# Kernel optimization log

Hardware: AMD Instinct MI355X
Metric: run time of the kernel (lower is better)

Reference implementation:

```python
import jax, jax.numpy as jnp
import numpy as np
import math

B, S, D, H = 4, 1024, 1024, 16
DK = D // H
WINDOW = 128
NEG = -100000.0


def setup_inputs() -> dict:
    key = jax.random.key(0)
    kx, kw1, kb1, kw2, kb2 = jax.random.split(key, 5)
    x = jax.random.normal(kx, (B, S, D), dtype=jnp.float32)
    # sliding-window band mask: True where |i-j| <= WINDOW
    i = jnp.arange(S)
    band = (jnp.abs(i[:, None] - i[None, :]) <= WINDOW)
    mask = jnp.broadcast_to(band, (B, S, S))
    # second structured mask: causal
    causal = (i[:, None] >= i[None, :])
    mask2 = jnp.broadcast_to(causal, (B, S, S))
    scale = 1.0 / math.sqrt(D)
    Wqkv = jax.random.normal(kw1, (D, 3 * D), dtype=jnp.float32) * scale
    bqkv = jax.random.normal(kb1, (3 * D,), dtype=jnp.float32) * 0.01
    Wo = jax.random.normal(kw2, (D, D), dtype=jnp.float32) * scale
    bo = jax.random.normal(kb2, (D,), dtype=jnp.float32) * 0.01
    return {"x": x, "mask": mask, "mask2": mask2, "Wqkv": Wqkv, "bqkv": bqkv, "Wo": Wo, "bo": bo}


def reference(x, mask, mask2, Wqkv, bqkv, Wo, bo):
    b, s, d = x.shape
    qkv = x @ Wqkv + bqkv                      # [b, s, 3d]
    q, k, v = jnp.split(qkv, 3, axis=-1)
    # [b, s, h, dk] -> [b, h, s, dk]
    q = q.reshape(b, s, H, DK).transpose(0, 2, 1, 3)
    k = k.reshape(b, s, H, DK).transpose(0, 2, 1, 3)
    v = v.reshape(b, s, H, DK).transpose(0, 2, 1, 3)
    scores = jnp.einsum('bhtd,bhsd->bhts', q, k) / math.sqrt(DK)
    scores = jnp.where(mask[:, None, :, :], scores, NEG)
    scores = jnp.where(mask2[:, None, :, :], scores, NEG)
    weights = jax.nn.softmax(scores, axis=-1)  # [b, h, t, s]
    context = jnp.einsum('bhts,bhsd->bhtd', weights, v)
    context = context.transpose(0, 2, 1, 3).reshape(b, s, d)
    context = context @ Wo + bo
    return (context, weights)
```

## Files before the change

### kernel.cpp

```cpp
#include <hip/hip_runtime.h>

typedef short bf16x8 __attribute__((ext_vector_type(8)));
typedef float floatx4 __attribute__((ext_vector_type(4)));

#define GLOBAL_AS __attribute__((address_space(1)))
#define LDS_AS __attribute__((address_space(3)))

__device__ __forceinline__ void gload_lds16(const ushort* g, ushort* l) {
  __builtin_amdgcn_global_load_lds((const GLOBAL_AS void*)g, (LDS_AS void*)l, 16, 0, 0);
}

__device__ __forceinline__ ushort f2bf(float x) {
  uint u = __float_as_uint(x);
  return (ushort)((u + 0x7fffu + ((u >> 16) & 1u)) >> 16);
}

__global__ __launch_bounds__(256) void k_f32_to_bf16(const float4* __restrict__ in,
                                                     ushort4* __restrict__ out, int n4) {
  int g = blockIdx.x * 256 + threadIdx.x;
  if (g < n4) {
    float4 v = in[g];
    ushort4 o;
    o.x = f2bf(v.x); o.y = f2bf(v.y); o.z = f2bf(v.z); o.w = f2bf(v.w);
    out[g] = o;
  }
}

__global__ __launch_bounds__(256) void k_transpose2(const float* __restrict__ W1,
                                                    ushort* __restrict__ O1,
                                                    const float* __restrict__ W2,
                                                    ushort* __restrict__ O2) {
  __shared__ float tile[32][33];
  int bx = blockIdx.x;
  const float* in; ushort* out; int N;
  if (bx < 96) { in = W1; out = O1; N = 3072; }
  else         { in = W2; out = O2; N = 1024; bx -= 96; }
  const int K = 1024;
  int n0 = bx * 32, k0 = blockIdx.y * 32;
  int tx = threadIdx.x & 31, ty = threadIdx.x >> 5;
  #pragma unroll
  for (int r = ty; r < 32; r += 8)
    tile[r][tx] = in[(size_t)(k0 + r) * N + n0 + tx];
  __syncthreads();
  #pragma unroll
  for (int r = ty; r < 32; r += 8)
    out[(size_t)(n0 + r) * K + k0 + tx] = f2bf(tile[tx][r]);
}

template <int OUT_BF16, int BN>
__global__ __launch_bounds__(256) void k_gemm_bt(const ushort* __restrict__ A,
                                                 const ushort* __restrict__ Bt,
                                                 const float* __restrict__ bias,
                                                 void* __restrict__ Cout,
                                                 int M, int N, int K) {
  constexpr int NI = BN / 32;
  constexpr int NB = BN / 64;
  __shared__ ushort As[128 * 32];
  __shared__ ushort Bs[BN * 32];
  const int t = threadIdx.x;
  const int m0 = blockIdx.y * 128, n0 = blockIdx.x * BN;
  const int w = t >> 6, l = t & 63;
  const int wm = (w & 1) * 64, wn = (w >> 1) * (BN / 2);
  const int lr = l & 15, q8 = (l >> 4) * 8;
  const int lrow = l >> 2, lcol = (l & 3) * 8;

  floatx4 acc[4][NI];
  #pragma unroll
  for (int i = 0; i < 4; ++i)
    #pragma unroll
    for (int j = 0; j < NI; ++j) acc[i][j] = (floatx4){0.f, 0.f, 0.f, 0.f};

  for (int k0 = 0; k0 < K; k0 += 32) {
    __syncthreads();
    #pragma unroll
    for (int i = 0; i < 2; ++i) {
      int r0 = (w * 2 + i) * 16;
      gload_lds16(A + (size_t)(m0 + r0 + lrow) * K + k0 + lcol, As + r0 * 32);
    }
    #pragma unroll
    for (int i = 0; i < NB; ++i) {
      int r0 = (w * NB + i) * 16;
      gload_lds16(Bt + (size_t)(n0 + r0 + lrow) * K + k0 + lcol, Bs + r0 * 32);
    }
    __syncthreads();
    bf16x8 af[4], bfr[NI];
    #pragma unroll
    for (int mi = 0; mi < 4; ++mi)
      af[mi] = *(const bf16x8*)(As + (wm + mi * 16 + lr) * 32 + q8);
    #pragma unroll
    for (int ni = 0; ni < NI; ++ni)
      bfr[ni] = *(const bf16x8*)(Bs + (wn + ni * 16 + lr) * 32 + q8);
    #pragma unroll
    for (int mi = 0; mi < 4; ++mi)
      #pragma unroll
      for (int ni = 0; ni < NI; ++ni)
        acc[mi][ni] = __builtin_amdgcn_mfma_f32_16x16x32_bf16(af[mi], bfr[ni], acc[mi][ni], 0, 0, 0);
  }

  const int rq = (l >> 4) * 4;
  #pragma unroll
  for (int ni = 0; ni < NI; ++ni) {
    int col = n0 + wn + ni * 16 + lr;
    float bv = bias[col];
    #pragma unroll
    for (int mi = 0; mi < 4; ++mi) {
      int row = m0 + wm + mi * 16 + rq;
      #pragma unroll
      for (int r2 = 0; r2 < 4; ++r2) {
        float v = acc[mi][ni][r2] + bv;
        size_t idx = (size_t)(row + r2) * N + col;
        if (OUT_BF16) ((ushort*)Cout)[idx] = f2bf(v);
        else          ((float*)Cout)[idx] = v;
      }
    }
  }
}

__global__ __launch_bounds__(256) void k_attn(const ushort* __restrict__ qkv,
                                              float* __restrict__ wout,
                                              ushort* __restrict__ ctxout) {
  __shared__ ushort smKP[192 * 68];
  __shared__ ushort smVT[64 * 200];
  __shared__ float smInv[64];

  const int t = threadIdx.x;
  const int w = t >> 6, l = t & 63;
  const int lr = l & 15, q8 = (l >> 4) * 8, q4 = (l >> 4) * 4;
  const int iblk = blockIdx.x & 15;
  const int h = (blockIdx.x >> 4) & 15;
  const int b = blockIdx.x >> 8;
  const int i0 = iblk * 64;
  const int jb0 = i0 - 128;
  const int tok0 = b * 1024 + i0;
  const int qoff = h * 64, koff = 1024 + h * 64, voff = 2048 + h * 64;
  const size_t wbase = ((size_t)(b * 16 + h) * 1024 + i0) * 1024;

  #pragma unroll
  for (int c = 0; c < 6; ++c) {
    int idx = t + 256 * c, row = idx >> 3, ch = idx & 7;
    int jsrc = jb0 + row; if (jsrc < 0) jsrc = 0;
    *(uint4*)(smKP + row * 68 + ch * 8) =
        *(const uint4*)(qkv + (size_t)(b * 1024 + jsrc) * 3072 + koff + ch * 8);
  }
  #pragma unroll
  for (int c = 0; c < 6; ++c) {
    int idx = t + 256 * c;
    int j = (idx & 15) + 16 * (idx >> 7);
    int d0 = ((idx >> 4) & 7) * 8;
    int jsrc = jb0 + j; if (jsrc < 0) jsrc = 0;
    uint4 u = *(const uint4*)(qkv + (size_t)(b * 1024 + jsrc) * 3072 + voff + d0);
    ushort* p = smVT + j;
    p[(d0 + 0) * 200] = (ushort)(u.x & 0xffffu);
    p[(d0 + 1) * 200] = (ushort)(u.x >> 16);
    p[(d0 + 2) * 200] = (ushort)(u.y & 0xffffu);
    p[(d0 + 3) * 200] = (ushort)(u.y >> 16);
    p[(d0 + 4) * 200] = (ushort)(u.z & 0xffffu);
    p[(d0 + 5) * 200] = (ushort)(u.z >> 16);
    p[(d0 + 6) * 200] = (ushort)(u.w & 0xffffu);
    p[(d0 + 7) * 200] = (ushort)(u.w >> 16);
  }

  const ushort* qrow = qkv + (size_t)(tok0 + w * 16 + lr) * 3072 + qoff;
  bf16x8 aq0 = *(const bf16x8*)(qrow + q8);
  bf16x8 aq1 = *(const bf16x8*)(qrow + 32 + q8);
  __syncthreads();

  floatx4 sc[12];
  #pragma unroll
  for (int ni = 0; ni < 12; ++ni) sc[ni] = (floatx4){0.f, 0.f, 0.f, 0.f};
  #pragma unroll
  for (int ni = 0; ni < 12; ++ni) {
    bf16x8 bk0 = *(const bf16x8*)(smKP + (ni * 16 + lr) * 68 + q8);
    bf16x8 bk1 = *(const bf16x8*)(smKP + (ni * 16 + lr) * 68 + 32 + q8);
    sc[ni] = __builtin_amdgcn_mfma_f32_16x16x32_bf16(aq0, bk0, sc[ni], 0, 0, 0);
    sc[ni] = __builtin_amdgcn_mfma_f32_16x16x32_bf16(aq1, bk1, sc[ni], 0, 0, 0);
  }
  __syncthreads();

  float mrow[4] = {-3e38f, -3e38f, -3e38f, -3e38f};
  #pragma unroll
  for (int ni = 0; ni < 12; ++ni) {
    int nj = ni * 16 + lr;
    #pragma unroll
    for (int reg = 0; reg < 4; ++reg) {
      int di = w * 16 + q4 + reg;
      bool valid = (nj >= di) & (nj <= di + 128) & (jb0 + nj >= 0);
      float s = valid ? sc[ni][reg] * 0.125f : -3e38f;
      sc[ni][reg] = s;
      mrow[reg] = fmaxf(mrow[reg], s);
    }
  }
  #pragma unroll
  for (int reg = 0; reg < 4; ++reg) {
    #pragma unroll
    for (int off = 1; off < 16; off <<= 1)
      mrow[reg] = fmaxf(mrow[reg], __shfl_xor(mrow[reg], off, 64));
  }
  float lrow[4] = {0.f, 0.f, 0.f, 0.f};
  #pragma unroll
  for (int ni = 0; ni < 12; ++ni) {
    #pragma unroll
    for (int reg = 0; reg < 4; ++reg) {
      float e = __expf(sc[ni][reg] - mrow[reg]);
      sc[ni][reg] = e;
      lrow[reg] += e;
    }
  }
  float inv[4];
  #pragma unroll
  for (int reg = 0; reg < 4; ++reg) {
    float s = lrow[reg];
    #pragma unroll
    for (int off = 1; off < 16; off <<= 1) s += __shfl_xor(s, off, 64);
    inv[reg] = 1.0f / s;
  }

  ushort* smP = smKP;
  #pragma unroll
  for (int ni = 0; ni < 12; ++ni) {
    int nj = ni * 16 + lr;
    #pragma unroll
    for (int reg = 0; reg < 4; ++reg) {
      int il = w * 16 + q4 + reg;
      smP[il * 204 + nj] = f2bf(sc[ni][reg]);
    }
  }
  if (lr == 0) {
    #pragma unroll
    for (int reg = 0; reg < 4; ++reg) smInv[w * 16 + q4 + reg] = inv[reg];
  }

  floatx4 oc[4];
  #pragma unroll
  for (int ni = 0; ni < 4; ++ni) oc[ni] = (floatx4){0.f, 0.f, 0.f, 0.f};
  #pragma unroll
  for (int ks = 0; ks < 6; ++ks) {
    bf16x8 ap = *(const bf16x8*)(smP + (w * 16 + lr) * 204 + ks * 32 + q8);
    #pragma unroll
    for (int ni = 0; ni < 4; ++ni) {
      bf16x8 bv = *(const bf16x8*)(smVT + (ni * 16 + lr) * 200 + ks * 32 + q8);
      oc[ni] = __builtin_amdgcn_mfma_f32_16x16x32_bf16(ap, bv, oc[ni], 0, 0, 0);
    }
  }

  #pragma unroll
  for (int ni = 0; ni < 4; ++ni) {
    int d = ni * 16 + lr;
    #pragma unroll
    for (int reg = 0; reg < 4; ++reg) {
      int il = w * 16 + q4 + reg;
      ctxout[(size_t)(tok0 + il) * 1024 + qoff + d] = f2bf(oc[ni][reg] * inv[reg]);
    }
  }

  __syncthreads();

  {
    const int j4 = t * 4;
    const unsigned nj4 = (unsigned)(j4 - jb0);
    const bool inband = nj4 < 192u;
    const int njc = inband ? (int)nj4 : 0;
    const float bandf = inband ? 1.0f : 0.0f;
    float* wp = wout + wbase + j4;
    const ushort* pp = smP + njc;
    #pragma unroll 4
    for (int r = 0; r < 64; ++r) {
      ushort4 pv = *(const ushort4*)(pp + r * 204);
      float iv = smInv[r] * bandf;
      floatx4 o = { __uint_as_float((uint)pv.x << 16) * iv,
                    __uint_as_float((uint)pv.y << 16) * iv,
                    __uint_as_float((uint)pv.z << 16) * iv,
                    __uint_as_float((uint)pv.w << 16) * iv };
      __builtin_nontemporal_store(o, (floatx4*)(wp + (size_t)r * 1024));
    }
  }
}

extern "C" void kernel_launch(void* const* d_in, const int* in_sizes, int n_in,
                              void* d_out, int out_size, void* d_ws, size_t ws_size,
                              hipStream_t stream) {
  const float* x    = (const float*)d_in[0];
  const float* Wqkv = (const float*)d_in[3];
  const float* bqkv = (const float*)d_in[4];
  const float* Wo   = (const float*)d_in[5];
  const float* bo   = (const float*)d_in[6];

  float* out_ctx = (float*)d_out;
  float* out_w   = out_ctx + (size_t)4 * 1024 * 1024;

  char* ws = (char*)d_ws;
  ushort* qkv_bf = (ushort*)(ws);
  ushort* ctx_bf = (ushort*)(ws + 25165824);
  ushort* x_bf   = (ushort*)(ws + 33554432);
  ushort* WqkvT  = (ushort*)(ws + 41943040);
  ushort* WoT    = (ushort*)(ws + 48234496);

  k_f32_to_bf16<<<4096, 256, 0, stream>>>((const float4*)x, (ushort4*)x_bf, 1048576);
  k_transpose2<<<dim3(128, 32), 256, 0, stream>>>(Wqkv, WqkvT, Wo, WoT);
  k_gemm_bt<1, 128><<<dim3(24, 32), 256, 0, stream>>>(x_bf, WqkvT, bqkv, qkv_bf, 4096, 3072, 1024);
  k_attn<<<1024, 256, 0, stream>>>(qkv_bf, out_w, ctx_bf);
  k_gemm_bt<0, 64><<<dim3(16, 32), 256, 0, stream>>>(ctx_bf, WoT, bo, out_ctx, 4096, 1024, 1024);
}
```

Measured before the change: 399.3 us.

## Pipeline GEMM loads through a 4-slot LDS ring with swizzle, fuse prep kernels

The GEMM now keeps four LDS buffers and issues global-to-LDS loads three K-tiles ahead. It waits with explicit vmcnt counts and uses a single barrier per iteration instead of two syncthreads. LDS columns are XOR-swizzled to cut bank conflicts on the fragment reads. The x conversion and weight transpose kernels are merged into one launch. The larger LDS footprint may reduce occupancy, and the manual waitcnt logic relies on the compiler's ordering of memory operations.

```diff
diff --git a/kernel.cpp b/kernel.cpp
--- a/kernel.cpp
+++ b/kernel.cpp
@@ -15,28 +15,26 @@
   return (ushort)((u + 0x7fffu + ((u >> 16) & 1u)) >> 16);
 }
 
-__global__ __launch_bounds__(256) void k_f32_to_bf16(const float4* __restrict__ in,
-                                                     ushort4* __restrict__ out, int n4) {
-  int g = blockIdx.x * 256 + threadIdx.x;
-  if (g < n4) {
-    float4 v = in[g];
+__global__ __launch_bounds__(256) void k_prep(const float4* __restrict__ x, ushort4* __restrict__ xbf,
+                                              const float* __restrict__ W1, ushort* __restrict__ O1,
+                                              const float* __restrict__ W2, ushort* __restrict__ O2) {
+  int bx = blockIdx.x;
+  if (bx < 4096) {
+    int g = bx * 256 + threadIdx.x;
+    float4 v = x[g];
     ushort4 o;
     o.x = f2bf(v.x); o.y = f2bf(v.y); o.z = f2bf(v.z); o.w = f2bf(v.w);
-    out[g] = o;
-  }
-}
-
-__global__ __launch_bounds__(256) void k_transpose2(const float* __restrict__ W1,
-                                                    ushort* __restrict__ O1,
-                                                    const float* __restrict__ W2,
-                                                    ushort* __restrict__ O2) {
+    xbf[g] = o;
+    return;
+  }
   __shared__ float tile[32][33];
-  int bx = blockIdx.x;
+  int tb = bx - 4096;
+  int by = tb >> 7, bxx = tb & 127;
   const float* in; ushort* out; int N;
-  if (bx < 96) { in = W1; out = O1; N = 3072; }
-  else         { in = W2; out = O2; N = 1024; bx -= 96; }
+  if (bxx < 96) { in = W1; out = O1; N = 3072; }
+  else          { in = W2; out = O2; N = 1024; bxx -= 96; }
   const int K = 1024;
-  int n0 = bx * 32, k0 = blockIdx.y * 32;
+  int n0 = bxx * 32, k0 = by * 32;
   int tx = threadIdx.x & 31, ty = threadIdx.x >> 5;
   #pragma unroll
   for (int r = ty; r < 32; r += 8)
@@ -48,21 +46,25 @@
 }
 
 template <int OUT_BF16, int BN>
-__global__ __launch_bounds__(256) void k_gemm_bt(const ushort* __restrict__ A,
-                                                 const ushort* __restrict__ Bt,
-                                                 const float* __restrict__ bias,
-                                                 void* __restrict__ Cout,
-                                                 int M, int N, int K) {
+__global__ __launch_bounds__(256) void k_gemm_ring(const ushort* __restrict__ A,
+                                                   const ushort* __restrict__ Bt,
+                                                   const float* __restrict__ bias,
+                                                   void* __restrict__ Cout,
+                                                   int M, int N, int K) {
   constexpr int NI = BN / 32;
   constexpr int NB = BN / 64;
-  __shared__ ushort As[128 * 32];
-  __shared__ ushort Bs[BN * 32];
+  constexpr int LOADS = 2 + NB;
+  __shared__ ushort As[4][128 * 32];
+  __shared__ ushort Bs[4][BN * 32];
   const int t = threadIdx.x;
   const int m0 = blockIdx.y * 128, n0 = blockIdx.x * BN;
   const int w = t >> 6, l = t & 63;
   const int wm = (w & 1) * 64, wn = (w >> 1) * (BN / 2);
-  const int lr = l & 15, q8 = (l >> 4) * 8;
-  const int lrow = l >> 2, lcol = (l & 3) * 8;
+  const int lr = l & 15;
+  const int lrow = l >> 2;
+  const int scol = ((l & 3) ^ ((l >> 3) & 3)) * 8;
+  const int swz = ((l >> 4) ^ ((lr >> 1) & 3)) * 8;
+  const int NT = K >> 5;
 
   floatx4 acc[4][NI];
   #pragma unroll
@@ -70,26 +72,38 @@
     #pragma unroll
     for (int j = 0; j < NI; ++j) acc[i][j] = (floatx4){0.f, 0.f, 0.f, 0.f};
 
-  for (int k0 = 0; k0 < K; k0 += 32) {
-    __syncthreads();
+  auto STAGE = [&](int slot, int k0) {
     #pragma unroll
     for (int i = 0; i < 2; ++i) {
       int r0 = (w * 2 + i) * 16;
-      gload_lds16(A + (size_t)(m0 + r0 + lrow) * K + k0 + lcol, As + r0 * 32);
+      gload_lds16(A + (size_t)(m0 + r0 + lrow) * K + k0 + scol, &As[slot][r0 * 32]);
     }
     #pragma unroll
     for (int i = 0; i < NB; ++i) {
       int r0 = (w * NB + i) * 16;
-      gload_lds16(Bt + (size_t)(n0 + r0 + lrow) * K + k0 + lcol, Bs + r0 * 32);
-    }
-    __syncthreads();
+      gload_lds16(Bt + (size_t)(n0 + r0 + lrow) * K + k0 + scol, &Bs[slot][r0 * 32]);
+    }
+  };
+
+  STAGE(0, 0);
+  STAGE(1, 32);
+  STAGE(2, 64);
+
+  for (int tt = 0; tt < NT; ++tt) {
+    if (tt + 2 < NT)      asm volatile("s_waitcnt vmcnt(%0)" :: "n"(2 * LOADS) : "memory");
+    else if (tt + 1 < NT) asm volatile("s_waitcnt vmcnt(%0)" :: "n"(LOADS) : "memory");
+    else                  asm volatile("s_waitcnt vmcnt(0)" ::: "memory");
+    __builtin_amdgcn_s_barrier();
+    if (tt + 3 < NT) STAGE((tt + 3) & 3, (tt + 3) * 32);
+    const ushort* as = &As[tt & 3][0];
+    const ushort* bs = &Bs[tt & 3][0];
     bf16x8 af[4], bfr[NI];
     #pragma unroll
     for (int mi = 0; mi < 4; ++mi)
-      af[mi] = *(const bf16x8*)(As + (wm + mi * 16 + lr) * 32 + q8);
+      af[mi] = *(const bf16x8*)(as + (wm + mi * 16 + lr) * 32 + swz);
     #pragma unroll
     for (int ni = 0; ni < NI; ++ni)
-      bfr[ni] = *(const bf16x8*)(Bs + (wn + ni * 16 + lr) * 32 + q8);
+      bfr[ni] = *(const bf16x8*)(bs + (wn + ni * 16 + lr) * 32 + swz);
     #pragma unroll
     for (int mi = 0; mi < 4; ++mi)
       #pragma unroll
@@ -295,9 +309,8 @@
   ushort* WqkvT  = (ushort*)(ws + 41943040);
   ushort* WoT    = (ushort*)(ws + 48234496);
 
-  k_f32_to_bf16<<<4096, 256, 0, stream>>>((const float4*)x, (ushort4*)x_bf, 1048576);
-  k_transpose2<<<dim3(128, 32), 256, 0, stream>>>(Wqkv, WqkvT, Wo, WoT);
-  k_gemm_bt<1, 128><<<dim3(24, 32), 256, 0, stream>>>(x_bf, WqkvT, bqkv, qkv_bf, 4096, 3072, 1024);
+  k_prep<<<8192, 256, 0, stream>>>((const float4*)x, (ushort4*)x_bf, Wqkv, WqkvT, Wo, WoT);
+  k_gemm_ring<1, 128><<<dim3(24, 32), 256, 0, stream>>>(x_bf, WqkvT, bqkv, qkv_bf, 4096, 3072, 1024);
   k_attn<<<1024, 256, 0, stream>>>(qkv_bf, out_w, ctx_bf);
-  k_gemm_bt<0, 64><<<dim3(16, 32), 256, 0, stream>>>(ctx_bf, WoT, bo, out_ctx, 4096, 1024, 1024);
-}
+  k_gemm_ring<0, 64><<<dim3(16, 32), 256, 0, stream>>>(ctx_bf, WoT, bo, out_ctx, 4096, 1024, 1024);
+}
```

Result: no change. 405.8 us (+1.6%).
